# Kernel tuning notes

Hardware: AMD Instinct MI355X
Metric: run time of the kernel (lower is better)

The kernel has to match this reference:

```python
import jax, jax.numpy as jnp
import numpy as np

FEAT_DIM = 384
HEAD_DIM = 32
N_HEADS = FEAT_DIM // HEAD_DIM
MAX_SEQ_LEN = 64
SIZE = 8  # sqrt(max_seq_len)


def _get_relative_position_index(height, width):
    coords_h = np.arange(height)
    coords_w = np.arange(width)
    coords = np.stack(np.meshgrid(coords_h, coords_w, indexing='ij'))
    coords_flat = coords.reshape(coords.shape[0], -1)
    relative_coords = coords_flat[:, :, None] - coords_flat[:, None, :]
    relative_coords = relative_coords.transpose(1, 2, 0)
    rh = relative_coords[:, :, 0] + (height - 1)
    rw = relative_coords[:, :, 1] + (width - 1)
    return jnp.asarray(rh * (2 * width - 1) + rw, dtype=jnp.int32)  # [P, P]


def setup_inputs() -> dict:
    key = jax.random.key(0)
    ks = jax.random.split(key, 6)
    B, G, P, D = 32, 64, MAX_SEQ_LEN, FEAT_DIM
    x = jax.random.normal(ks[0], (B, G, P, D), dtype=jnp.float32)
    qkv_w = jax.random.normal(ks[1], (D, 3 * D), dtype=jnp.float32) * (1.0 / np.sqrt(D))
    qkv_b = jnp.zeros((3 * D,), dtype=jnp.float32)
    merge_w = jax.random.normal(ks[2], (D, D), dtype=jnp.float32) * (1.0 / np.sqrt(D))
    merge_b = jnp.zeros((D,), dtype=jnp.float32)
    n_bias = (2 * SIZE - 1) * (2 * SIZE - 1)  # 225
    bias_table = jax.random.truncated_normal(ks[3], -2.0, 2.0, (n_bias, N_HEADS), dtype=jnp.float32) * 0.02
    rel_index = _get_relative_position_index(SIZE, SIZE)
    return {"x": x, "qkv_w": qkv_w, "qkv_b": qkv_b, "merge_w": merge_w,
            "merge_b": merge_b, "bias_table": bias_table, "rel_index": rel_index}


def reference(x, qkv_w, qkv_b, merge_w, merge_b, bias_table, rel_index):
    B, G, P, D = x.shape
    H, DH = N_HEADS, HEAD_DIM
    scale = 1.0 / np.sqrt(D)  # NOTE: module scales by feat_dim**-0.5, not head_dim
    qkv = x @ qkv_w + qkv_b  # [B,G,P,3D]
    q, k, v = jnp.split(qkv, 3, axis=-1)
    q = q.reshape(B, G, P, H, DH).transpose(0, 1, 3, 2, 4)  # [B,G,H,P,DH]
    k = k.reshape(B, G, P, H, DH).transpose(0, 1, 3, 2, 4)
    v = v.reshape(B, G, P, H, DH).transpose(0, 1, 3, 2, 4)
    scores = jnp.einsum('bghid,bghjd->bghij', q, k * scale)  # [B,G,H,P,P]
    pos_bias = bias_table[rel_index.reshape(-1)].reshape(P, P, H)
    pos_bias = pos_bias.transpose(2, 0, 1)[None, None]  # [1,1,H,P,P]
    attn = jax.nn.softmax(scores + pos_bias, axis=-1)
    out = jnp.einsum('bghij,bghjd->bghid', attn, v)  # [B,G,H,P,DH]
    out = out.transpose(0, 1, 3, 2, 4).reshape(B, G, P, D)
    return out @ merge_w + merge_b
```

## Files before the change

kernel.cpp:

```cpp
#include <hip/hip_runtime.h>
#include <hip/hip_bf16.h>
#include <cstdint>
#include <cstddef>


typedef __bf16 bf16_t;
typedef __bf16 bf16x8 __attribute__((ext_vector_type(8)));
typedef float  f32x4  __attribute__((ext_vector_type(4)));

#define MFMA16(A, B, C) __builtin_amdgcn_mfma_f32_16x16x32_bf16((A), (B), (C), 0, 0, 0)

#define NBLK   2048
#define SCALE  0.051031036307982884f
#define LOG2E  1.4426950408889634f

#define BAR()  do { asm volatile("s_waitcnt lgkmcnt(0)" ::: "memory"); \
                    __builtin_amdgcn_s_barrier(); } while (0)
#define BARV() do { asm volatile("s_waitcnt vmcnt(0) lgkmcnt(0)" ::: "memory"); \
                    __builtin_amdgcn_s_barrier(); } while (0)

__device__ __forceinline__ void gld_lds16(const bf16_t* g, bf16_t* l) {
  __builtin_amdgcn_global_load_lds(
      (const __attribute__((address_space(1))) void*)g,
      (__attribute__((address_space(3))) void*)l, 16, 0, 0);
}


__global__ void prep_kernel(const float* __restrict__ qkv_w,
                            const float* __restrict__ qkv_b,
                            const float* __restrict__ merge_w,
                            const float* __restrict__ bias_table,
                            const int*   __restrict__ rel_index,
                            bf16_t* __restrict__ qkv_wT,
                            bf16_t* __restrict__ merge_wT,
                            bf16_t* __restrict__ biasx,
                            float*  __restrict__ qkvb_s) {
  int idx = blockIdx.x * 256 + threadIdx.x;
  if (idx < 1152 * 384) {
    int n = idx / 384, k = idx - n * 384;
    float v = qkv_w[k * 1152 + n];
    if (n >= 384 && n < 768) v *= SCALE;
    qkv_wT[idx] = (bf16_t)v;
    return;
  }
  int i2 = idx - 1152 * 384;
  if (i2 < 384 * 384) {
    int n = i2 / 384, k = i2 - n * 384;
    merge_wT[i2] = (bf16_t)merge_w[k * 384 + n];
    return;
  }
  int i3 = i2 - 384 * 384;
  if (i3 < 12 * 64 * 64) {
    int h = i3 / 4096, r = i3 - h * 4096;
    biasx[i3] = (bf16_t)bias_table[rel_index[r] * 12 + h];
    return;
  }
  int i4 = i3 - 12 * 64 * 64;
  if (i4 < 1152) {
    float v = qkv_b[i4];
    if (i4 >= 384 && i4 < 768) v *= SCALE;
    qkvb_s[i4] = v;
  }
}

__global__ void __launch_bounds__(256)
convert_x(const float* __restrict__ x, bf16_t* __restrict__ xb) {
  int hc = blockIdx.x * 256 + threadIdx.x;
  int br = hc / 48;
  int ch = hc - br * 48;
  int row = br & 63;
  const float4* xg = (const float4*)x;
  float4 v0 = xg[hc * 2];
  float4 v1 = xg[hc * 2 + 1];
  union { bf16_t b[8]; uint4 u; } pk;
  pk.b[0] = (bf16_t)v0.x; pk.b[1] = (bf16_t)v0.y;
  pk.b[2] = (bf16_t)v0.z; pk.b[3] = (bf16_t)v0.w;
  pk.b[4] = (bf16_t)v1.x; pk.b[5] = (bf16_t)v1.y;
  pk.b[6] = (bf16_t)v1.z; pk.b[7] = (bf16_t)v1.w;
  ((uint4*)xb)[br * 48 + (ch ^ (row & 7))] = pk.u;
}

__device__ inline float bflo(unsigned u) {
  union { unsigned x; float f; } v; v.x = u << 16; return v.f;
}
__device__ inline float bfhi(unsigned u) {
  union { unsigned x; float f; } v; v.x = u & 0xffff0000u; return v.f;
}

__global__ void __launch_bounds__(512, 4)
fused_qkv_attn(const bf16_t* __restrict__ xbf,
               const bf16_t* __restrict__ wT,
               const float*  __restrict__ qbias,
               const bf16_t* __restrict__ biasx,
               bf16_t* __restrict__ attn) {
  extern __shared__ char smem_raw[];
  bf16_t* lds = (bf16_t*)smem_raw;
  bf16_t* xs  = lds;
  bf16_t* qs  = lds;
  bf16_t* ks  = lds + 8192;
  bf16_t* vts = lds + 16384;
  bf16_t* ps  = lds + 24576;

  const int tid  = threadIdx.x;
  const int blk  = blockIdx.x;
  const int lane = tid & 63;
  const int w    = tid >> 6;
  const int c    = lane & 15;
  const int g    = lane >> 4;
  const int cx   = c & 7;

  const f32x4 zf = {0.f, 0.f, 0.f, 0.f};
  const bf16_t* xg = xbf + (size_t)blk * 24576;

#pragma unroll 1
  for (int pass = 0; pass < 3; ++pass) {
    BAR();

#pragma unroll
    for (int it = 0; it < 6; ++it) {
      int e = (tid + it * 512) * 8;
      gld_lds16(xg + e, xs + e);
    }
    BARV();

    f32x4 acc[3][4];
#pragma unroll
    for (int t = 0; t < 3; ++t)
#pragma unroll
      for (int mt = 0; mt < 4; ++mt) acc[t][mt] = zf;

    int nrow[3];
    const bf16_t* wp[3];
    float bv[3];
#pragma unroll
    for (int t = 0; t < 3; ++t) {
      int tau  = w * 3 + t;
      int kind = tau >> 3;
      int u    = tau & 7;
      nrow[t]  = kind * 384 + (pass * 4 + (u >> 1)) * 32 + (u & 1) * 16;
      wp[t]    = wT + (size_t)(nrow[t] + c) * 384 + g * 8;
      bv[t]    = qbias[nrow[t] + c];
    }
    bf16x8 bc[3], bn[3];
#pragma unroll
    for (int t = 0; t < 3; ++t) bc[t] = *(const bf16x8*)(wp[t]);
#pragma unroll
    for (int k = 0; k < 12; ++k) {
      if (k < 11) {
#pragma unroll
        for (int t = 0; t < 3; ++t) bn[t] = *(const bf16x8*)(wp[t] + (k + 1) * 32);
      }
      int chv = (((4 * k + g) ^ cx) << 3);
#pragma unroll
      for (int mt = 0; mt < 4; ++mt) {
        bf16x8 a = *(const bf16x8*)(xs + (mt * 16 + c) * 384 + chv);
#pragma unroll
        for (int t = 0; t < 3; ++t)
          acc[t][mt] = MFMA16(a, bc[t], acc[t][mt]);
      }
#pragma unroll
      for (int t = 0; t < 3; ++t) bc[t] = bn[t];
    }

    BAR();

#pragma unroll
    for (int t = 0; t < 3; ++t) {
      int tau  = w * 3 + t;
      int kind = tau >> 3;
      int u    = tau & 7;
      int hl   = u >> 1, c16 = u & 1;
      if (kind == 2) {
        int d = c16 * 16 + c;
        bf16_t* vbase = vts + hl * 2048 + d * 64;
#pragma unroll
        for (int mt = 0; mt < 4; ++mt) {
          union { bf16_t b[4]; uint2 u2; } pk;
#pragma unroll
          for (int r = 0; r < 4; ++r) pk.b[r] = (bf16_t)(acc[t][mt][r] + bv[t]);
          int chunk = (2 * mt + (g >> 1)) ^ cx;
          *(uint2*)(vbase + chunk * 8 + (g & 1) * 4) = pk.u2;
        }
      } else {
        int f  = c16 * 16 + c;
        int fc = f >> 3;
        int fl = f & 7;
        bf16_t* dst = (kind == 0 ? qs : ks) + hl * 2048;
#pragma unroll
        for (int mt = 0; mt < 4; ++mt)
#pragma unroll
          for (int r = 0; r < 4; ++r)
            dst[(mt * 16 + g * 4 + r) * 32 + ((fc ^ g) << 3) + fl] =
                (bf16_t)(acc[t][mt][r] + bv[t]);
      }
    }
    BAR();

    {
      const int hl = w >> 1, ih = w & 1;
      const int h  = pass * 4 + hl;
      const int rsw = (c >> 2) & 3;

      f32x4 sacc[4][2];
#pragma unroll
      for (int mt = 0; mt < 4; ++mt)
#pragma unroll
        for (int nt = 0; nt < 2; ++nt) sacc[mt][nt] = zf;
      bf16x8 ka[4], qf[2];
#pragma unroll
      for (int mt = 0; mt < 4; ++mt)
        ka[mt] = *(const bf16x8*)(ks + hl * 2048 + (mt * 16 + c) * 32 +
                                  ((g ^ rsw) << 3));
#pragma unroll
      for (int nt = 0; nt < 2; ++nt)
        qf[nt] = *(const bf16x8*)(qs + hl * 2048 + (ih * 32 + nt * 16 + c) * 32 +
                                  ((g ^ rsw) << 3));
#pragma unroll
      for (int mt = 0; mt < 4; ++mt)
#pragma unroll
        for (int nt = 0; nt < 2; ++nt)
          sacc[mt][nt] = MFMA16(ka[mt], qf[nt], sacc[mt][nt]);

      const bf16_t* bp = biasx + h * 4096;
      float mx[2] = {-3.0e38f, -3.0e38f};
#pragma unroll
      for (int nt = 0; nt < 2; ++nt) {
        int i = ih * 32 + nt * 16 + c;
#pragma unroll
        for (int mt = 0; mt < 4; ++mt) {
          uint2 bb = *(const uint2*)(bp + i * 64 + mt * 16 + g * 4);
          sacc[mt][nt][0] += bflo(bb.x);
          sacc[mt][nt][1] += bfhi(bb.x);
          sacc[mt][nt][2] += bflo(bb.y);
          sacc[mt][nt][3] += bfhi(bb.y);
          mx[nt] = fmaxf(mx[nt], fmaxf(fmaxf(sacc[mt][nt][0], sacc[mt][nt][1]),
                                       fmaxf(sacc[mt][nt][2], sacc[mt][nt][3])));
        }
      }
#pragma unroll
      for (int nt = 0; nt < 2; ++nt) {
        mx[nt] = fmaxf(mx[nt], __shfl_xor(mx[nt], 16));
        mx[nt] = fmaxf(mx[nt], __shfl_xor(mx[nt], 32));
      }

      bf16_t* psw = ps + w * 1024;
      bf16x8 va[2][2];
#pragma unroll
      for (int m2 = 0; m2 < 2; ++m2)
#pragma unroll
        for (int kt = 0; kt < 2; ++kt)
          va[m2][kt] = *(const bf16x8*)(vts + hl * 2048 + (m2 * 16 + c) * 64 +
                                        (((4 * kt + g) ^ cx) << 3));
      f32x4 oacc[2][2];
#pragma unroll
      for (int m2 = 0; m2 < 2; ++m2)
#pragma unroll
        for (int nt = 0; nt < 2; ++nt) oacc[m2][nt] = zf;

      float l[2] = {0.f, 0.f};
#pragma unroll
      for (int nt = 0; nt < 2; ++nt) {
#pragma unroll
        for (int mt = 0; mt < 4; ++mt) {
          float p0 = exp2f((sacc[mt][nt][0] - mx[nt]) * LOG2E);
          float p1 = exp2f((sacc[mt][nt][1] - mx[nt]) * LOG2E);
          float p2 = exp2f((sacc[mt][nt][2] - mx[nt]) * LOG2E);
          float p3 = exp2f((sacc[mt][nt][3] - mx[nt]) * LOG2E);
          l[nt] += (p0 + p1) + (p2 + p3);
          union { bf16_t b[4]; uint2 u2; } pk;
          pk.b[0] = (bf16_t)p0; pk.b[1] = (bf16_t)p1;
          pk.b[2] = (bf16_t)p2; pk.b[3] = (bf16_t)p3;
          int chunk = (2 * mt + (g >> 1)) ^ cx;
          *(uint2*)(psw + c * 64 + chunk * 8 + (g & 1) * 4) = pk.u2;
        }
        bf16x8 pb[2];
#pragma unroll
        for (int kt = 0; kt < 2; ++kt)
          pb[kt] = *(const bf16x8*)(psw + c * 64 + (((4 * kt + g) ^ cx) << 3));
#pragma unroll
        for (int m2 = 0; m2 < 2; ++m2)
#pragma unroll
          for (int kt = 0; kt < 2; ++kt)
            oacc[m2][nt] = MFMA16(va[m2][kt], pb[kt], oacc[m2][nt]);
      }

#pragma unroll
      for (int nt = 0; nt < 2; ++nt) {
        l[nt] += __shfl_xor(l[nt], 16);
        l[nt] += __shfl_xor(l[nt], 32);
      }

#pragma unroll
      for (int nt = 0; nt < 2; ++nt) {
        float inv = 1.0f / l[nt];
        int row = blk * 64 + ih * 32 + nt * 16 + c;
#pragma unroll
        for (int m2 = 0; m2 < 2; ++m2) {
          union { bf16_t b[4]; uint2 u2; } pk;
#pragma unroll
          for (int r = 0; r < 4; ++r) pk.b[r] = (bf16_t)(oacc[m2][nt][r] * inv);
          *(uint2*)(attn + (size_t)row * 384 + h * 32 + m2 * 16 + g * 4) = pk.u2;
        }
      }
    }
  }
}

#define XS 408
__global__ void __launch_bounds__(512)
merge_gemm(const bf16_t* __restrict__ attn,
           const bf16_t* __restrict__ mwT,
           const float*  __restrict__ mb,
           float* __restrict__ out) {
  __shared__ bf16_t as[64 * XS];
  const int tid = threadIdx.x, blk = blockIdx.x;
  const int lane = tid & 63, w = tid >> 6, c = lane & 15, g = lane >> 4;

  {
    const int4* ag = (const int4*)(attn + (size_t)blk * (64 * 384));
#pragma unroll
    for (int it = 0; it < 6; ++it) {
      int idx = tid + it * 512;
      int row = idx / 48;
      int col = (idx - row * 48) * 8;
      *(int4*)(as + row * XS + col) = ag[idx];
    }
  }
  __syncthreads();

  const f32x4 zf = {0.f, 0.f, 0.f, 0.f};
  f32x4 acc[3][4];
#pragma unroll
  for (int t = 0; t < 3; ++t)
#pragma unroll
    for (int mt = 0; mt < 4; ++mt) acc[t][mt] = zf;

  const int n0 = w * 48;
  const bf16_t* wp[3];
#pragma unroll
  for (int t = 0; t < 3; ++t) wp[t] = mwT + (size_t)(n0 + t * 16 + c) * 384 + g * 8;
  bf16x8 bc[3], bn[3];
#pragma unroll
  for (int t = 0; t < 3; ++t) bc[t] = *(const bf16x8*)(wp[t]);
#pragma unroll
  for (int k = 0; k < 12; ++k) {
    if (k < 11) {
#pragma unroll
      for (int t = 0; t < 3; ++t) bn[t] = *(const bf16x8*)(wp[t] + (k + 1) * 32);
    }
    bf16x8 a[4];
#pragma unroll
    for (int mt = 0; mt < 4; ++mt)
      a[mt] = *(const bf16x8*)(as + (mt * 16 + c) * XS + k * 32 + g * 8);
#pragma unroll
    for (int t = 0; t < 3; ++t)
#pragma unroll
      for (int mt = 0; mt < 4; ++mt)
        acc[t][mt] = MFMA16(a[mt], bc[t], acc[t][mt]);
#pragma unroll
    for (int t = 0; t < 3; ++t) bc[t] = bn[t];
  }

#pragma unroll
  for (int t = 0; t < 3; ++t) {
    float bias = mb[n0 + t * 16 + c];
#pragma unroll
    for (int mt = 0; mt < 4; ++mt)
#pragma unroll
      for (int r = 0; r < 4; ++r)
        out[(size_t)(blk * 64 + mt * 16 + g * 4 + r) * 384 + n0 + t * 16 + c] =
            acc[t][mt][r] + bias;
  }
}

extern "C" void kernel_launch(void* const* d_in, const int* in_sizes, int n_in,
                              void* d_out, int out_size, void* d_ws, size_t ws_size,
                              hipStream_t stream) {
  const float* x          = (const float*)d_in[0];
  const float* qkv_w      = (const float*)d_in[1];
  const float* qkv_b      = (const float*)d_in[2];
  const float* merge_w    = (const float*)d_in[3];
  const float* merge_b    = (const float*)d_in[4];
  const float* bias_table = (const float*)d_in[5];
  const int*   rel_index  = (const int*)d_in[6];
  float*       out        = (float*)d_out;

  const size_t OFF_QKVWT = 0;
  const size_t OFF_MWT   = 884736;
  const size_t OFF_BIAS  = OFF_MWT + 294912;
  const size_t OFF_QB    = OFF_BIAS + 98304;
  const size_t OFF_ATTN  = OFF_QB + 4608;
  const size_t NEED      = OFF_ATTN + (size_t)100663296;
  if (ws_size < NEED) return;

  char* ws = (char*)d_ws;
  bf16_t* qkv_wT  = (bf16_t*)(ws + OFF_QKVWT);
  bf16_t* mwT     = (bf16_t*)(ws + OFF_MWT);
  bf16_t* biasx   = (bf16_t*)(ws + OFF_BIAS);
  float*  qkvb_s  = (float*)(ws + OFF_QB);
  bf16_t* attnbuf = (bf16_t*)(ws + OFF_ATTN);
  bf16_t* xbf     = (bf16_t*)d_out;

  prep_kernel<<<2501, 256, 0, stream>>>(qkv_w, qkv_b, merge_w, bias_table,
                                        rel_index, qkv_wT, mwT, biasx, qkvb_s);

  convert_x<<<24576, 256, 0, stream>>>(x, xbf);

  hipFuncSetAttribute(reinterpret_cast<const void*>(fused_qkv_attn),
                      hipFuncAttributeMaxDynamicSharedMemorySize, 65536);
  fused_qkv_attn<<<NBLK, 512, 65536, stream>>>(xbf, qkv_wT, qkvb_s, biasx, attnbuf);

  merge_gemm<<<NBLK, 512, 0, stream>>>(attnbuf, mwT, merge_b, out);
}
```

Baseline: 494.4 us.

## Load x fragments directly from global into registers, shrink LDS footprint

The QKV projection now reads its A-operand fragments straight from global memory into registers with software prefetch, instead of staging the 64x384 x tile into LDS with global_load_lds each pass. The x swizzle in convert_x is removed, the probability buffer is aliased onto the Q region, and a barrier is added after the score MFMAs so that aliasing stays safe. Dynamic LDS drops from 64KB to 48KB, which can allow more resident blocks per CU. In exchange, each pass re-reads x from global/L2 with 16-byte per-lane loads, which are less coalesced than the old staged copy.

```diff
diff --git a/kernel.cpp b/kernel.cpp
--- a/kernel.cpp
+++ b/kernel.cpp
@@ -16,14 +16,6 @@
 
 #define BAR()  do { asm volatile("s_waitcnt lgkmcnt(0)" ::: "memory"); \
                     __builtin_amdgcn_s_barrier(); } while (0)
-#define BARV() do { asm volatile("s_waitcnt vmcnt(0) lgkmcnt(0)" ::: "memory"); \
-                    __builtin_amdgcn_s_barrier(); } while (0)
-
-__device__ __forceinline__ void gld_lds16(const bf16_t* g, bf16_t* l) {
-  __builtin_amdgcn_global_load_lds(
-      (const __attribute__((address_space(1))) void*)g,
-      (__attribute__((address_space(3))) void*)l, 16, 0, 0);
-}
 
 
 __global__ void prep_kernel(const float* __restrict__ qkv_w,
@@ -66,9 +58,6 @@
 __global__ void __launch_bounds__(256)
 convert_x(const float* __restrict__ x, bf16_t* __restrict__ xb) {
   int hc = blockIdx.x * 256 + threadIdx.x;
-  int br = hc / 48;
-  int ch = hc - br * 48;
-  int row = br & 63;
   const float4* xg = (const float4*)x;
   float4 v0 = xg[hc * 2];
   float4 v1 = xg[hc * 2 + 1];
@@ -77,7 +66,7 @@
   pk.b[2] = (bf16_t)v0.z; pk.b[3] = (bf16_t)v0.w;
   pk.b[4] = (bf16_t)v1.x; pk.b[5] = (bf16_t)v1.y;
   pk.b[6] = (bf16_t)v1.z; pk.b[7] = (bf16_t)v1.w;
-  ((uint4*)xb)[br * 48 + (ch ^ (row & 7))] = pk.u;
+  ((uint4*)xb)[hc] = pk.u;
 }
 
 __device__ inline float bflo(unsigned u) {
@@ -95,11 +84,10 @@
                bf16_t* __restrict__ attn) {
   extern __shared__ char smem_raw[];
   bf16_t* lds = (bf16_t*)smem_raw;
-  bf16_t* xs  = lds;
   bf16_t* qs  = lds;
   bf16_t* ks  = lds + 8192;
   bf16_t* vts = lds + 16384;
-  bf16_t* ps  = lds + 24576;
+  bf16_t* ps  = lds;
 
   const int tid  = threadIdx.x;
   const int blk  = blockIdx.x;
@@ -114,15 +102,6 @@
 
 #pragma unroll 1
   for (int pass = 0; pass < 3; ++pass) {
-    BAR();
-
-#pragma unroll
-    for (int it = 0; it < 6; ++it) {
-      int e = (tid + it * 512) * 8;
-      gld_lds16(xg + e, xs + e);
-    }
-    BARV();
-
     f32x4 acc[3][4];
 #pragma unroll
     for (int t = 0; t < 3; ++t)
@@ -141,25 +120,32 @@
       wp[t]    = wT + (size_t)(nrow[t] + c) * 384 + g * 8;
       bv[t]    = qbias[nrow[t] + c];
     }
-    bf16x8 bc[3], bn[3];
-#pragma unroll
-    for (int t = 0; t < 3; ++t) bc[t] = *(const bf16x8*)(wp[t]);
+    const bf16_t* ap[4];
+#pragma unroll
+    for (int mt = 0; mt < 4; ++mt) ap[mt] = xg + (mt * 16 + c) * 384 + g * 8;
+
+    bf16x8 bc[3], bn[3], ac[4], an[4];
+#pragma unroll
+    for (int t = 0; t < 3; ++t)  bc[t] = *(const bf16x8*)(wp[t]);
+#pragma unroll
+    for (int mt = 0; mt < 4; ++mt) ac[mt] = *(const bf16x8*)(ap[mt]);
 #pragma unroll
     for (int k = 0; k < 12; ++k) {
       if (k < 11) {
 #pragma unroll
-        for (int t = 0; t < 3; ++t) bn[t] = *(const bf16x8*)(wp[t] + (k + 1) * 32);
-      }
-      int chv = (((4 * k + g) ^ cx) << 3);
-#pragma unroll
-      for (int mt = 0; mt < 4; ++mt) {
-        bf16x8 a = *(const bf16x8*)(xs + (mt * 16 + c) * 384 + chv);
-#pragma unroll
-        for (int t = 0; t < 3; ++t)
-          acc[t][mt] = MFMA16(a, bc[t], acc[t][mt]);
-      }
-#pragma unroll
-      for (int t = 0; t < 3; ++t) bc[t] = bn[t];
+        for (int t = 0; t < 3; ++t)  bn[t] = *(const bf16x8*)(wp[t] + (k + 1) * 32);
+#pragma unroll
+        for (int mt = 0; mt < 4; ++mt) an[mt] = *(const bf16x8*)(ap[mt] + (k + 1) * 32);
+      }
+#pragma unroll
+      for (int t = 0; t < 3; ++t)
+#pragma unroll
+        for (int mt = 0; mt < 4; ++mt)
+          acc[t][mt] = MFMA16(ac[mt], bc[t], acc[t][mt]);
+#pragma unroll
+      for (int t = 0; t < 3; ++t)  bc[t] = bn[t];
+#pragma unroll
+      for (int mt = 0; mt < 4; ++mt) ac[mt] = an[mt];
     }
 
     BAR();
@@ -201,12 +187,7 @@
       const int h  = pass * 4 + hl;
       const int rsw = (c >> 2) & 3;
 
-      f32x4 sacc[4][2];
-#pragma unroll
-      for (int mt = 0; mt < 4; ++mt)
-#pragma unroll
-        for (int nt = 0; nt < 2; ++nt) sacc[mt][nt] = zf;
-      bf16x8 ka[4], qf[2];
+      bf16x8 ka[4], qf[2], va[2][2];
 #pragma unroll
       for (int mt = 0; mt < 4; ++mt)
         ka[mt] = *(const bf16x8*)(ks + hl * 2048 + (mt * 16 + c) * 32 +
@@ -216,10 +197,24 @@
         qf[nt] = *(const bf16x8*)(qs + hl * 2048 + (ih * 32 + nt * 16 + c) * 32 +
                                   ((g ^ rsw) << 3));
 #pragma unroll
+      for (int m2 = 0; m2 < 2; ++m2)
+#pragma unroll
+        for (int kt = 0; kt < 2; ++kt)
+          va[m2][kt] = *(const bf16x8*)(vts + hl * 2048 + (m2 * 16 + c) * 64 +
+                                        (((4 * kt + g) ^ cx) << 3));
+
+      f32x4 sacc[4][2];
+#pragma unroll
+      for (int mt = 0; mt < 4; ++mt)
+#pragma unroll
+        for (int nt = 0; nt < 2; ++nt) sacc[mt][nt] = zf;
+#pragma unroll
       for (int mt = 0; mt < 4; ++mt)
 #pragma unroll
         for (int nt = 0; nt < 2; ++nt)
           sacc[mt][nt] = MFMA16(ka[mt], qf[nt], sacc[mt][nt]);
+
+      BAR();
 
       const bf16_t* bp = biasx + h * 4096;
       float mx[2] = {-3.0e38f, -3.0e38f};
@@ -244,13 +239,6 @@
       }
 
       bf16_t* psw = ps + w * 1024;
-      bf16x8 va[2][2];
-#pragma unroll
-      for (int m2 = 0; m2 < 2; ++m2)
-#pragma unroll
-        for (int kt = 0; kt < 2; ++kt)
-          va[m2][kt] = *(const bf16x8*)(vts + hl * 2048 + (m2 * 16 + c) * 64 +
-                                        (((4 * kt + g) ^ cx) << 3));
       f32x4 oacc[2][2];
 #pragma unroll
       for (int m2 = 0; m2 < 2; ++m2)
@@ -407,8 +395,8 @@
   convert_x<<<24576, 256, 0, stream>>>(x, xbf);
 
   hipFuncSetAttribute(reinterpret_cast<const void*>(fused_qkv_attn),
-                      hipFuncAttributeMaxDynamicSharedMemorySize, 65536);
-  fused_qkv_attn<<<NBLK, 512, 65536, stream>>>(xbf, qkv_wT, qkvb_s, biasx, attnbuf);
+                      hipFuncAttributeMaxDynamicSharedMemorySize, 49152);
+  fused_qkv_attn<<<NBLK, 512, 49152, stream>>>(xbf, qkv_wT, qkvb_s, biasx, attnbuf);
 
   merge_gemm<<<NBLK, 512, 0, stream>>>(attnbuf, mwT, merge_b, out);
 }
```

Result: slower. 1.002 ms (+102.6%).
